# Kernel tuning notes

Measured on AMD Instinct MI355X. Metric: run time of the kernel, lower is better.

## Reference

```python
import jax, jax.numpy as jnp
import numpy as np
from jax import lax

THRESHOLD = 0.7
OUT = 224  # output size of nn.Upsample(size=(224,224), mode='bilinear', align_corners=True)


def _bilinear(img, xs, ys):
    """align_corners=True bilinear sampling. img: (..., H, W); xs: (oh,), ys: (ow,) float coords."""
    H, W = img.shape[-2], img.shape[-1]
    x0 = jnp.clip(jnp.floor(xs).astype(jnp.int32), 0, H - 1)
    x1 = jnp.clip(x0 + 1, 0, H - 1)
    y0 = jnp.clip(jnp.floor(ys).astype(jnp.int32), 0, W - 1)
    y1 = jnp.clip(y0 + 1, 0, W - 1)
    wx = (xs - x0.astype(xs.dtype))[:, None]  # (oh,1)
    wy = (ys - y0.astype(ys.dtype))[None, :]  # (1,ow)
    top = jnp.take(img, x0, axis=-2)
    bot = jnp.take(img, x1, axis=-2)
    v00 = jnp.take(top, y0, axis=-1)
    v01 = jnp.take(top, y1, axis=-1)
    v10 = jnp.take(bot, y0, axis=-1)
    v11 = jnp.take(bot, y1, axis=-1)
    return (1 - wx) * ((1 - wy) * v00 + wy * v01) + wx * ((1 - wy) * v10 + wy * v11)


def _normalize01(h):
    n = h.shape[0]
    f = h.reshape(n, -1)
    mn = f.min(axis=1, keepdims=True)
    mx = f.max(axis=1, keepdims=True)
    return ((f - mn) / (mx - mn)).reshape(h.shape)


def _largest_cc(mask):
    """8-connected (skimage connectivity=2) largest component via min-label propagation.
    mask: (N,H,W) bool -> (N,H,W) bool, True on the largest connected component."""
    N, H, W = mask.shape
    BIG = H * W  # background sentinel label
    idx = jnp.arange(BIG, dtype=jnp.int32).reshape(1, H, W)
    lab0 = jnp.where(mask, idx, BIG)

    def body(state):
        lab, _ = state
        pooled = lax.reduce_window(lab, jnp.int32(BIG), lax.min, (1, 3, 3), (1, 1, 1), 'SAME')
        new = jnp.where(mask, pooled, BIG)
        return new, jnp.any(new != lab)

    lab, _ = lax.while_loop(lambda s: s[1], body, (lab0, jnp.bool_(True)))

    def counts(l):
        return jnp.zeros(BIG + 1, jnp.int32).at[l.reshape(-1)].add(1)

    c = jax.vmap(counts)(lab)                 # (N, H*W+1); last bin = background
    best = jnp.argmax(c[:, :BIG], axis=1)     # label of largest foreground component
    return lab == best[:, None, None]


def _bbox(lcc):
    N, H, W = lcc.shape
    rows = lcc.any(axis=2)
    cols = lcc.any(axis=1)
    has = rows.any(axis=1)
    xmin = jnp.argmax(rows, axis=1).astype(jnp.int32)
    xmax = (H - 1 - jnp.argmax(rows[:, ::-1], axis=1)).astype(jnp.int32)
    ymin = jnp.argmax(cols, axis=1).astype(jnp.int32)
    ymax = (W - 1 - jnp.argmax(cols[:, ::-1], axis=1)).astype(jnp.int32)
    # fallback to full image if the mask is empty (torch code would crash here)
    xmin = jnp.where(has, xmin, 0)
    ymin = jnp.where(has, ymin, 0)
    xmax = jnp.where(has, xmax, H - 1)
    ymax = jnp.where(has, ymax, W - 1)
    return xmin, xmax, ymin, ymax


def _crop_resize(images, xmin, xmax, ymin, ymax):
    # torch crop is images[i][:, xmin:xmax, ymin:ymax] (exclusive upper), then align_corners resize
    grid = jnp.arange(OUT, dtype=jnp.float32) / (OUT - 1)

    def one(img, a, b, c, d):
        Lx = jnp.maximum(b - a, 1)
        Ly = jnp.maximum(d - c, 1)
        xs = a.astype(jnp.float32) + grid * (Lx - 1).astype(jnp.float32)
        ys = c.astype(jnp.float32) + grid * (Ly - 1).astype(jnp.float32)
        return _bilinear(img, xs, ys)

    return jax.vmap(one)(images, xmin, xmax, ymin, ymax)


def setup_inputs() -> dict:
    key = jax.random.key(0)
    k1, k2 = jax.random.split(key)
    x = jax.random.normal(k1, (64, 3, 224, 224), dtype=jnp.float32)
    features = jax.random.normal(k2, (64, 2048, 7, 7), dtype=jnp.float32)
    return {"x": x, "features": features}


def reference(x, features):
    # distance = normalize01(Lmax(features, axis=1))
    heat = _normalize01(jnp.max(jnp.abs(features), axis=1))       # (N, h, w)
    h, w = heat.shape[1], heat.shape[2]
    grid = jnp.arange(OUT, dtype=jnp.float32) / (OUT - 1)
    out_heatmap = _bilinear(heat, grid * (h - 1), grid * (w - 1))  # (N, 224, 224)
    mask = out_heatmap > THRESHOLD
    lcc = _largest_cc(mask)
    xmin, xmax, ymin, ymax = _bbox(lcc)
    crop = _crop_resize(x, xmin, xmax, ymin, ymax)                 # (N, 3, 224, 224)
    coords = jnp.stack([ymin, xmin, ymax, xmax], axis=1)           # (N, 4), torch coord order
    return crop, out_heatmap, coords
```

## Files before the change

### kernel.cpp

```cpp
#include <hip/hip_runtime.h>
#include <stdint.h>

#define NIMG   64
#define NCH    2048
#define HW7    49
#define OUTW   224
#define NPIX   50176
#define CROP_N 9633792
#define HEAT_OFF  9633792
#define COORD_OFF 12845056
#define THRESH 0.7f

#define MAXR 4
#define RCAP (224*MAXR)
#define NWORDS 784
#define WPAD   788

#define NGRP 16

#define MASKW_BYTE_OFF 262144
#define CNT_BYTE_OFF   663552

__global__ __launch_bounds__(256) void k1_heat(const float* __restrict__ F,
                                               float* __restrict__ heatPart,
                                               unsigned* __restrict__ imgCnt) {
    __shared__ float smax[4][64];
    const int t = threadIdx.x;
    const int b = blockIdx.x;
    if (b == 0 && t < NIMG) {
        __hip_atomic_store(&imgCnt[t], 0u, __ATOMIC_RELAXED, __HIP_MEMORY_SCOPE_AGENT);
    }
    const int n = b >> 4, g = b & 15;
    const int w = t >> 6, l = t & 63;
    const int lp = (l < HW7) ? l : 0;
    const float* base = F + (size_t)n * 100352 + (size_t)(g * 128 + w) * HW7 + lp;
    float vmax = 0.0f;
#pragma unroll 8
    for (int i = 0; i < 32; ++i) {
        vmax = fmaxf(vmax, fabsf(base[(size_t)i * 4 * HW7]));
    }
    smax[w][l] = vmax;
    __syncthreads();
    if (t < HW7) {
        float m = fmaxf(fmaxf(smax[0][t], smax[1][t]), fmaxf(smax[2][t], smax[3][t]));
        heatPart[b * HW7 + t] = m;
    }
}

__device__ inline unsigned uf_find(volatile unsigned* P, unsigned x) {
    while (true) {
        unsigned p = P[x];
        if (p == x) return x;
        unsigned gp = P[p];
        if (gp == p) return p;
        P[x] = gp;
        x = gp;
    }
}

__device__ inline void uf_merge(volatile unsigned* P, unsigned a, unsigned b) {
    while (true) {
        a = uf_find(P, a); b = uf_find(P, b);
        if (a == b) return;
        if (a > b) { unsigned tmp = a; a = b; b = tmp; }
        unsigned old = atomicCAS((unsigned*)&P[b], b, a);
        if (old == b) return;
        b = old;
    }
}

__global__ __launch_bounds__(1024) void k23_heatmask(const float* __restrict__ heatPart,
                                                     float* __restrict__ heatOut,
                                                     unsigned long long* __restrict__ maskW,
                                                     unsigned* __restrict__ imgCnt,
                                                     float* __restrict__ coords) {
#pragma clang fp contract(off)
    __shared__ float raw[HW7];
    __shared__ float h7[HW7];
    __shared__ float s_mn, s_mx;
    __shared__ float wT[OUTW];
    __shared__ int   i0T[OUTW];
    __shared__ int   i1T[OUTW];
    __shared__ int   s_last;
    __shared__ unsigned long long W[WPAD];
    __shared__ unsigned short runS[RCAP], runE[RCAP];
    __shared__ unsigned char nRuns[224];
    __shared__ unsigned parent[RCAP], cnt[RCAP];
    __shared__ unsigned rmin[RCAP], rmax[RCAP], cmin[RCAP], cmax[RCAP];
    __shared__ unsigned bestScore, bestRid;

    const int t = threadIdx.x;
    const int b = blockIdx.x;
    const int n = b >> 2, slice = b & 3;

    if (t < HW7) {
        float m = heatPart[(n * NGRP + 0) * HW7 + t];
#pragma unroll
        for (int g = 1; g < NGRP; ++g) m = fmaxf(m, heatPart[(n * NGRP + g) * HW7 + t]);
        raw[t] = m;
    }
    if (t < OUTW) {
        float gx = (float)t / 223.0f;
        float xs = gx * 6.0f;
        int x0 = (int)floorf(xs); x0 = min(max(x0, 0), 6);
        i0T[t] = x0;
        i1T[t] = min(x0 + 1, 6);
        wT[t]  = xs - (float)x0;
    }
    __syncthreads();
    if (t == 0) {
        float mn = raw[0], mx = raw[0];
        for (int i = 1; i < HW7; ++i) { float v = raw[i]; mn = fminf(mn, v); mx = fmaxf(mx, v); }
        s_mn = mn; s_mx = mx;
    }
    __syncthreads();
    if (t < HW7) h7[t] = (raw[t] - s_mn) / (s_mx - s_mn);
    __syncthreads();

    const int pbase = slice * 12544;
    for (int k = 0; k < 13; ++k) {
        int pl = (k << 10) + t;
        if (pl < 12544) {
            int p = pbase + pl;
            int i = p / 224, j = p - i * 224;
            int x0 = i0T[i], x1 = i1T[i];
            int y0 = i0T[j], y1 = i1T[j];
            float wx = wT[i], wy = wT[j];
            float v00 = h7[x0 * 7 + y0], v01 = h7[x0 * 7 + y1];
            float v10 = h7[x1 * 7 + y0], v11 = h7[x1 * 7 + y1];
            float val = (1.0f - wx) * ((1.0f - wy) * v00 + wy * v01)
                      + wx * ((1.0f - wy) * v10 + wy * v11);
            heatOut[(size_t)n * NPIX + p] = val;
            unsigned long long bal = __ballot(val > THRESH);
            if ((t & 63) == 0) {
                __hip_atomic_store(&maskW[(size_t)n * NWORDS + (p >> 6)], bal,
                                   __ATOMIC_RELAXED, __HIP_MEMORY_SCOPE_AGENT);
            }
        }
    }

    __syncthreads();
    if (t == 0) {
        unsigned old = __hip_atomic_fetch_add(&imgCnt[n], 1u,
                                              __ATOMIC_ACQ_REL, __HIP_MEMORY_SCOPE_AGENT);
        s_last = (old == 3u);
    }
    __syncthreads();
    if (!s_last) return;

    if (t < NWORDS) W[t] = __hip_atomic_load(&maskW[(size_t)n * NWORDS + t],
                                             __ATOMIC_RELAXED, __HIP_MEMORY_SCOPE_AGENT);
    if (t >= NWORDS && t < WPAD) W[t] = 0ull;
    if (t < RCAP) {
        parent[t] = (unsigned)t; cnt[t] = 0u;
        rmin[t] = 0xFFFFFFFFu; rmax[t] = 0u; cmin[t] = 0xFFFFFFFFu; cmax[t] = 0u;
    }
    if (t == 0) { bestScore = 0u; bestRid = 0u; }
    __syncthreads();

    if (t < 224) {
        const int r = t;
        const int bit0 = r * 224;
        const int w0 = bit0 >> 6, sh = bit0 & 63;
        unsigned long long rb[4];
#pragma unroll
        for (int q = 0; q < 4; ++q) {
            unsigned long long lo = W[w0 + q] >> sh;
            unsigned long long hi = sh ? (W[w0 + q + 1] << (64 - sh)) : 0ull;
            rb[q] = lo | hi;
        }
        rb[3] &= 0xFFFFFFFFull;

        unsigned long long st[4], en[4];
        unsigned long long carry = 0ull;
#pragma unroll
        for (int q = 0; q < 4; ++q) {
            unsigned long long shl = (rb[q] << 1) | carry;
            carry = rb[q] >> 63;
            st[q] = rb[q] & ~shl;
        }
#pragma unroll
        for (int q = 0; q < 4; ++q) {
            unsigned long long nxt = (q < 3) ? rb[q + 1] : 0ull;
            en[q] = rb[q] & ~((rb[q] >> 1) | (nxt << 63));
        }
        int ns = 0;
#pragma unroll
        for (int q = 0; q < 4; ++q) {
            unsigned long long x = st[q];
            while (x) {
                int z = __builtin_ctzll(x); x &= x - 1;
                if (ns < MAXR) runS[r * MAXR + ns] = (unsigned short)(q * 64 + z);
                ns++;
            }
        }
        int ne = 0;
#pragma unroll
        for (int q = 0; q < 4; ++q) {
            unsigned long long x = en[q];
            while (x) {
                int z = __builtin_ctzll(x); x &= x - 1;
                if (ne < MAXR) runE[r * MAXR + ne] = (unsigned short)(q * 64 + z);
                ne++;
            }
        }
        nRuns[r] = (unsigned char)min(ns, MAXR);
    }
    __syncthreads();

    if (t >= MAXR && t < RCAP) {
        const int r = t >> 2, k = t & (MAXR - 1);
        if (k < (int)nRuns[r]) {
            const int nb = nRuns[r - 1];
            int s = runS[t], e = runE[t];
            for (int m = 0; m < nb; ++m) {
                int qid = (r - 1) * MAXR + m;
                int s2 = runS[qid], e2 = runE[qid];
                if (s2 <= e + 1 && e2 >= s - 1) uf_merge(parent, (unsigned)t, (unsigned)qid);
            }
        }
    }
    __syncthreads();

    if (t < RCAP) {
        int r = t >> 2, k = t & (MAXR - 1);
        if (k < (int)nRuns[r]) {
            int s = runS[t], e = runE[t];
            unsigned root = uf_find(parent, (unsigned)t);
            atomicAdd(&cnt[root], (unsigned)(e - s + 1));
            atomicMin(&rmin[root], (unsigned)r);
            atomicMax(&rmax[root], (unsigned)r);
            atomicMin(&cmin[root], (unsigned)s);
            atomicMax(&cmax[root], (unsigned)e);
        }
    }
    __syncthreads();

    if (t < RCAP) {
        unsigned c = cnt[t];
        if (c > 0u) {
            unsigned label = (unsigned)((t >> 2) * 224 + (int)runS[t]);
            unsigned score = (c << 16) | (65535u - label);
            atomicMax(&bestScore, score);
        }
    }
    __syncthreads();
    if (t < RCAP) {
        unsigned c = cnt[t];
        if (c > 0u) {
            unsigned label = (unsigned)((t >> 2) * 224 + (int)runS[t]);
            unsigned score = (c << 16) | (65535u - label);
            if (score == bestScore) bestRid = (unsigned)t;
        }
    }
    __syncthreads();

    if (t == 0) {
        int xmin, xmax, ymin, ymax;
        if (bestScore == 0u) {
            xmin = 0; ymin = 0; xmax = 223; ymax = 223;
        } else {
            unsigned rb_ = bestRid;
            xmin = (int)rmin[rb_]; xmax = (int)rmax[rb_];
            ymin = (int)cmin[rb_]; ymax = (int)cmax[rb_];
        }
        coords[n * 4 + 0] = (float)ymin;
        coords[n * 4 + 1] = (float)xmin;
        coords[n * 4 + 2] = (float)ymax;
        coords[n * 4 + 3] = (float)xmax;
    }
}

__global__ __launch_bounds__(256) void k4_crop(const float* __restrict__ X,
                                               const float* __restrict__ coords,
                                               float* __restrict__ out) {
#pragma clang fp contract(off)
    const int t = threadIdx.x;
    const int b = blockIdx.x;
    const int n = b / 49;
    const int p4 = ((b % 49) * 256 + t) * 4;
    const int oi = p4 / 224, oj = p4 - oi * 224;

    int ymin = (int)coords[n * 4 + 0];
    int xmin = (int)coords[n * 4 + 1];
    int ymax = (int)coords[n * 4 + 2];
    int xmax = (int)coords[n * 4 + 3];
    int Lx = max(xmax - xmin, 1);
    int Ly = max(ymax - ymin, 1);

    float gx = (float)oi / 223.0f;
    float xs = (float)xmin + gx * (float)(Lx - 1);
    int x0 = (int)floorf(xs); x0 = min(max(x0, 0), 223); int x1 = min(x0 + 1, 223);
    float wx = xs - (float)x0;

    int   y0q[4], y1q[4];
    float wyq[4];
#pragma unroll
    for (int q = 0; q < 4; ++q) {
        float gy = (float)(oj + q) / 223.0f;
        float ys = (float)ymin + gy * (float)(Ly - 1);
        int y0 = (int)floorf(ys); y0 = min(max(y0, 0), 223);
        y0q[q] = y0; y1q[q] = min(y0 + 1, 223);
        wyq[q] = ys - (float)y0;
    }

    const float* img = X + (size_t)n * 150528;
    float* obase = out + (size_t)n * 150528 + p4;
#pragma unroll
    for (int ch = 0; ch < 3; ++ch) {
        const float* rt = img + ch * NPIX + x0 * 224;
        const float* rb = img + ch * NPIX + x1 * 224;
        float r[4];
#pragma unroll
        for (int q = 0; q < 4; ++q) {
            float v00 = rt[y0q[q]], v01 = rt[y1q[q]];
            float v10 = rb[y0q[q]], v11 = rb[y1q[q]];
            r[q] = (1.0f - wx) * ((1.0f - wyq[q]) * v00 + wyq[q] * v01)
                 + wx * ((1.0f - wyq[q]) * v10 + wyq[q] * v11);
        }
        *reinterpret_cast<float4*>(obase + (size_t)ch * NPIX) =
            make_float4(r[0], r[1], r[2], r[3]);
    }
}

extern "C" void kernel_launch(void* const* d_in, const int* in_sizes, int n_in,
                              void* d_out, int out_size, void* d_ws, size_t ws_size,
                              hipStream_t stream) {
    (void)in_sizes; (void)n_in; (void)out_size; (void)d_ws; (void)ws_size;
    const float* X = (const float*)d_in[0];
    const float* F = (const float*)d_in[1];
    float* out = (float*)d_out;

    float* heatPart = (float*)d_out;
    unsigned long long* maskW = (unsigned long long*)((char*)d_out + MASKW_BYTE_OFF);
    unsigned* imgCnt = (unsigned*)((char*)d_out + CNT_BYTE_OFF);
    float* heatOut = out + HEAT_OFF;
    float* coords  = out + COORD_OFF;

    k1_heat     <<<dim3(1024), dim3(256),  0, stream>>>(F, heatPart, imgCnt);
    k23_heatmask<<<dim3(256),  dim3(1024), 0, stream>>>(heatPart, heatOut, maskW, imgCnt, coords);
    k4_crop     <<<dim3(3136), dim3(256),  0, stream>>>(X, coords, out);
}
```

Measured before the change: 137.5 us.

## Fuse heatmap, connected-component and crop stages into one kernel with flag sync

Merges the heat/mask kernel and the crop-resize kernel into a single 256-block kernel. The last block per image computes the bbox and publishes a flag, and the other three slice blocks spin-wait on that flag before doing their share of the crop. Scratch buffers move from the output buffer to the workspace when one is available, and the old three-kernel path is kept as a fallback. This removes one kernel launch and its boundary, but adds a spin-wait that assumes all 256 blocks of 1024 threads are co-resident, and the crop runs on only 256 blocks instead of 3136.

```diff
diff --git a/kernel.cpp b/kernel.cpp
--- a/kernel.cpp
+++ b/kernel.cpp
@@ -18,8 +18,13 @@
 
 #define NGRP 16
 
-#define MASKW_BYTE_OFF 262144
-#define CNT_BYTE_OFF   663552
+#define WS_HP_OFF    0
+#define WS_MW_OFF    200704
+#define WS_CNT_OFF   602112
+#define WS_NEEDED    602624
+
+#define FB_MASKW_BYTE_OFF 262144
+#define FB_CNT_BYTE_OFF   663552
 
 __global__ __launch_bounds__(256) void k1_heat(const float* __restrict__ F,
                                                float* __restrict__ heatPart,
@@ -27,7 +32,7 @@
     __shared__ float smax[4][64];
     const int t = threadIdx.x;
     const int b = blockIdx.x;
-    if (b == 0 && t < NIMG) {
+    if (b == 0 && t < 128) {
         __hip_atomic_store(&imgCnt[t], 0u, __ATOMIC_RELAXED, __HIP_MEMORY_SCOPE_AGENT);
     }
     const int n = b >> 4, g = b & 15;
@@ -66,6 +71,275 @@
         unsigned old = atomicCAS((unsigned*)&P[b], b, a);
         if (old == b) return;
         b = old;
+    }
+}
+
+__global__ __launch_bounds__(1024) void k234(const float* __restrict__ heatPart,
+                                             const float* __restrict__ X,
+                                             unsigned long long* __restrict__ maskW,
+                                             unsigned* __restrict__ cnt1,
+                                             unsigned* __restrict__ flag,
+                                             float* heatOut,
+                                             float* coords,
+                                             float* out) {
+#pragma clang fp contract(off)
+    __shared__ float raw[HW7];
+    __shared__ float h7[HW7];
+    __shared__ float s_mn, s_mx;
+    __shared__ float wT[OUTW];
+    __shared__ int   i0T[OUTW];
+    __shared__ int   i1T[OUTW];
+    __shared__ int   s_last;
+    __shared__ unsigned long long W[WPAD];
+    __shared__ unsigned short runS[RCAP], runE[RCAP];
+    __shared__ unsigned char nRuns[224];
+    __shared__ unsigned parent[RCAP], cnt[RCAP];
+    __shared__ unsigned rmin[RCAP], rmax[RCAP], cmin[RCAP], cmax[RCAP];
+    __shared__ unsigned bestScore, bestRid;
+    __shared__ float s_crd[4];
+
+    const int t = threadIdx.x;
+    const int b = blockIdx.x;
+    const int n = b >> 2, slice = b & 3;
+
+    if (t < HW7) {
+        float m = heatPart[(n * NGRP + 0) * HW7 + t];
+#pragma unroll
+        for (int g = 1; g < NGRP; ++g) m = fmaxf(m, heatPart[(n * NGRP + g) * HW7 + t]);
+        raw[t] = m;
+    }
+    if (t < OUTW) {
+        float gx = (float)t / 223.0f;
+        float xs = gx * 6.0f;
+        int x0 = (int)floorf(xs); x0 = min(max(x0, 0), 6);
+        i0T[t] = x0;
+        i1T[t] = min(x0 + 1, 6);
+        wT[t]  = xs - (float)x0;
+    }
+    __syncthreads();
+    if (t == 0) {
+        float mn = raw[0], mx = raw[0];
+        for (int i = 1; i < HW7; ++i) { float v = raw[i]; mn = fminf(mn, v); mx = fmaxf(mx, v); }
+        s_mn = mn; s_mx = mx;
+    }
+    __syncthreads();
+    if (t < HW7) h7[t] = (raw[t] - s_mn) / (s_mx - s_mn);
+    __syncthreads();
+
+    const int pbase = slice * 12544;
+    for (int k = 0; k < 13; ++k) {
+        int pl = (k << 10) + t;
+        if (pl < 12544) {
+            int p = pbase + pl;
+            int i = p / 224, j = p - i * 224;
+            int x0 = i0T[i], x1 = i1T[i];
+            int y0 = i0T[j], y1 = i1T[j];
+            float wx = wT[i], wy = wT[j];
+            float v00 = h7[x0 * 7 + y0], v01 = h7[x0 * 7 + y1];
+            float v10 = h7[x1 * 7 + y0], v11 = h7[x1 * 7 + y1];
+            float val = (1.0f - wx) * ((1.0f - wy) * v00 + wy * v01)
+                      + wx * ((1.0f - wy) * v10 + wy * v11);
+            heatOut[(size_t)n * NPIX + p] = val;
+            unsigned long long bal = __ballot(val > THRESH);
+            if ((t & 63) == 0) {
+                __hip_atomic_store(&maskW[(size_t)n * NWORDS + (p >> 6)], bal,
+                                   __ATOMIC_RELAXED, __HIP_MEMORY_SCOPE_AGENT);
+            }
+        }
+    }
+
+    __syncthreads();
+    if (t == 0) {
+        unsigned old = __hip_atomic_fetch_add(&cnt1[n], 1u,
+                                              __ATOMIC_ACQ_REL, __HIP_MEMORY_SCOPE_AGENT);
+        s_last = (old == 3u);
+    }
+    __syncthreads();
+
+    if (s_last) {
+        if (t < NWORDS) W[t] = __hip_atomic_load(&maskW[(size_t)n * NWORDS + t],
+                                                 __ATOMIC_RELAXED, __HIP_MEMORY_SCOPE_AGENT);
+        if (t >= NWORDS && t < WPAD) W[t] = 0ull;
+        if (t < RCAP) {
+            parent[t] = (unsigned)t; cnt[t] = 0u;
+            rmin[t] = 0xFFFFFFFFu; rmax[t] = 0u; cmin[t] = 0xFFFFFFFFu; cmax[t] = 0u;
+        }
+        if (t == 0) { bestScore = 0u; bestRid = 0u; }
+        __syncthreads();
+
+        if (t < 224) {
+            const int r = t;
+            const int bit0 = r * 224;
+            const int w0 = bit0 >> 6, sh = bit0 & 63;
+            unsigned long long rb[4];
+#pragma unroll
+            for (int q = 0; q < 4; ++q) {
+                unsigned long long lo = W[w0 + q] >> sh;
+                unsigned long long hi = sh ? (W[w0 + q + 1] << (64 - sh)) : 0ull;
+                rb[q] = lo | hi;
+            }
+            rb[3] &= 0xFFFFFFFFull;
+
+            unsigned long long st[4], en[4];
+            unsigned long long carry = 0ull;
+#pragma unroll
+            for (int q = 0; q < 4; ++q) {
+                unsigned long long shl = (rb[q] << 1) | carry;
+                carry = rb[q] >> 63;
+                st[q] = rb[q] & ~shl;
+            }
+#pragma unroll
+            for (int q = 0; q < 4; ++q) {
+                unsigned long long nxt = (q < 3) ? rb[q + 1] : 0ull;
+                en[q] = rb[q] & ~((rb[q] >> 1) | (nxt << 63));
+            }
+            int ns = 0;
+#pragma unroll
+            for (int q = 0; q < 4; ++q) {
+                unsigned long long x = st[q];
+                while (x) {
+                    int z = __builtin_ctzll(x); x &= x - 1;
+                    if (ns < MAXR) runS[r * MAXR + ns] = (unsigned short)(q * 64 + z);
+                    ns++;
+                }
+            }
+            int ne = 0;
+#pragma unroll
+            for (int q = 0; q < 4; ++q) {
+                unsigned long long x = en[q];
+                while (x) {
+                    int z = __builtin_ctzll(x); x &= x - 1;
+                    if (ne < MAXR) runE[r * MAXR + ne] = (unsigned short)(q * 64 + z);
+                    ne++;
+                }
+            }
+            nRuns[r] = (unsigned char)min(ns, MAXR);
+        }
+        __syncthreads();
+
+        if (t >= MAXR && t < RCAP) {
+            const int r = t >> 2, k = t & (MAXR - 1);
+            if (k < (int)nRuns[r]) {
+                const int nb = nRuns[r - 1];
+                int s = runS[t], e = runE[t];
+                for (int m = 0; m < nb; ++m) {
+                    int qid = (r - 1) * MAXR + m;
+                    int s2 = runS[qid], e2 = runE[qid];
+                    if (s2 <= e + 1 && e2 >= s - 1) uf_merge(parent, (unsigned)t, (unsigned)qid);
+                }
+            }
+        }
+        __syncthreads();
+
+        if (t < RCAP) {
+            int r = t >> 2, k = t & (MAXR - 1);
+            if (k < (int)nRuns[r]) {
+                int s = runS[t], e = runE[t];
+                unsigned root = uf_find(parent, (unsigned)t);
+                atomicAdd(&cnt[root], (unsigned)(e - s + 1));
+                atomicMin(&rmin[root], (unsigned)r);
+                atomicMax(&rmax[root], (unsigned)r);
+                atomicMin(&cmin[root], (unsigned)s);
+                atomicMax(&cmax[root], (unsigned)e);
+            }
+        }
+        __syncthreads();
+
+        if (t < RCAP) {
+            unsigned c = cnt[t];
+            if (c > 0u) {
+                unsigned label = (unsigned)((t >> 2) * 224 + (int)runS[t]);
+                unsigned score = (c << 16) | (65535u - label);
+                atomicMax(&bestScore, score);
+            }
+        }
+        __syncthreads();
+        if (t < RCAP) {
+            unsigned c = cnt[t];
+            if (c > 0u) {
+                unsigned label = (unsigned)((t >> 2) * 224 + (int)runS[t]);
+                unsigned score = (c << 16) | (65535u - label);
+                if (score == bestScore) bestRid = (unsigned)t;
+            }
+        }
+        __syncthreads();
+
+        if (t == 0) {
+            int xmin, xmax, ymin, ymax;
+            if (bestScore == 0u) {
+                xmin = 0; ymin = 0; xmax = 223; ymax = 223;
+            } else {
+                unsigned rb_ = bestRid;
+                xmin = (int)rmin[rb_]; xmax = (int)rmax[rb_];
+                ymin = (int)cmin[rb_]; ymax = (int)cmax[rb_];
+            }
+            __hip_atomic_store(&coords[n * 4 + 0], (float)ymin, __ATOMIC_RELAXED, __HIP_MEMORY_SCOPE_AGENT);
+            __hip_atomic_store(&coords[n * 4 + 1], (float)xmin, __ATOMIC_RELAXED, __HIP_MEMORY_SCOPE_AGENT);
+            __hip_atomic_store(&coords[n * 4 + 2], (float)ymax, __ATOMIC_RELAXED, __HIP_MEMORY_SCOPE_AGENT);
+            __hip_atomic_store(&coords[n * 4 + 3], (float)xmax, __ATOMIC_RELAXED, __HIP_MEMORY_SCOPE_AGENT);
+            __hip_atomic_store(&flag[n], 1u, __ATOMIC_RELEASE, __HIP_MEMORY_SCOPE_AGENT);
+        }
+    }
+
+    if (t == 0) {
+        while (__hip_atomic_load(&flag[n], __ATOMIC_ACQUIRE, __HIP_MEMORY_SCOPE_AGENT) == 0u) {
+            __builtin_amdgcn_s_sleep(2);
+        }
+    }
+    __syncthreads();
+    if (t < 4) s_crd[t] = __hip_atomic_load(&coords[n * 4 + t],
+                                            __ATOMIC_RELAXED, __HIP_MEMORY_SCOPE_AGENT);
+    __syncthreads();
+
+    {
+        const int ymin = (int)s_crd[0];
+        const int xmin = (int)s_crd[1];
+        const int ymax = (int)s_crd[2];
+        const int xmax = (int)s_crd[3];
+        const int Lx = max(xmax - xmin, 1);
+        const int Ly = max(ymax - ymin, 1);
+        const float* img = X + (size_t)n * 150528;
+
+        for (int iter = 0; iter < 4; ++iter) {
+            int loc = (iter << 10) + t;
+            if (loc < 3136) {
+                int p4 = (slice * 3136 + loc) * 4;
+                int oi = p4 / 224, oj = p4 - oi * 224;
+
+                float gx = (float)oi / 223.0f;
+                float xs = (float)xmin + gx * (float)(Lx - 1);
+                int x0 = (int)floorf(xs); x0 = min(max(x0, 0), 223); int x1 = min(x0 + 1, 223);
+                float wx = xs - (float)x0;
+
+                int   y0q[4], y1q[4];
+                float wyq[4];
+#pragma unroll
+                for (int q = 0; q < 4; ++q) {
+                    float gy = (float)(oj + q) / 223.0f;
+                    float ys = (float)ymin + gy * (float)(Ly - 1);
+                    int y0 = (int)floorf(ys); y0 = min(max(y0, 0), 223);
+                    y0q[q] = y0; y1q[q] = min(y0 + 1, 223);
+                    wyq[q] = ys - (float)y0;
+                }
+
+                float* obase = out + (size_t)n * 150528 + p4;
+#pragma unroll
+                for (int ch = 0; ch < 3; ++ch) {
+                    const float* rt = img + ch * NPIX + x0 * 224;
+                    const float* rb = img + ch * NPIX + x1 * 224;
+                    float r[4];
+#pragma unroll
+                    for (int q = 0; q < 4; ++q) {
+                        float v00 = rt[y0q[q]], v01 = rt[y1q[q]];
+                        float v10 = rb[y0q[q]], v11 = rb[y1q[q]];
+                        r[q] = (1.0f - wx) * ((1.0f - wyq[q]) * v00 + wyq[q] * v01)
+                             + wx * ((1.0f - wyq[q]) * v10 + wyq[q] * v11);
+                    }
+                    *reinterpret_cast<float4*>(obase + (size_t)ch * NPIX) =
+                        make_float4(r[0], r[1], r[2], r[3]);
+                }
+            }
+        }
     }
 }
 
@@ -170,7 +444,6 @@
             rb[q] = lo | hi;
         }
         rb[3] &= 0xFFFFFFFFull;
-
         unsigned long long st[4], en[4];
         unsigned long long carry = 0ull;
 #pragma unroll
@@ -326,18 +599,29 @@
 extern "C" void kernel_launch(void* const* d_in, const int* in_sizes, int n_in,
                               void* d_out, int out_size, void* d_ws, size_t ws_size,
                               hipStream_t stream) {
-    (void)in_sizes; (void)n_in; (void)out_size; (void)d_ws; (void)ws_size;
+    (void)in_sizes; (void)n_in; (void)out_size;
     const float* X = (const float*)d_in[0];
     const float* F = (const float*)d_in[1];
     float* out = (float*)d_out;
-
-    float* heatPart = (float*)d_out;
-    unsigned long long* maskW = (unsigned long long*)((char*)d_out + MASKW_BYTE_OFF);
-    unsigned* imgCnt = (unsigned*)((char*)d_out + CNT_BYTE_OFF);
     float* heatOut = out + HEAT_OFF;
     float* coords  = out + COORD_OFF;
 
-    k1_heat     <<<dim3(1024), dim3(256),  0, stream>>>(F, heatPart, imgCnt);
-    k23_heatmask<<<dim3(256),  dim3(1024), 0, stream>>>(heatPart, heatOut, maskW, imgCnt, coords);
-    k4_crop     <<<dim3(3136), dim3(256),  0, stream>>>(X, coords, out);
+    if (d_ws != nullptr && ws_size >= (size_t)WS_NEEDED) {
+        float* heatPart = (float*)((char*)d_ws + WS_HP_OFF);
+        unsigned long long* maskW = (unsigned long long*)((char*)d_ws + WS_MW_OFF);
+        unsigned* cnt1 = (unsigned*)((char*)d_ws + WS_CNT_OFF);
+        unsigned* flag = cnt1 + 64;
+
+        k1_heat<<<dim3(1024), dim3(256),  0, stream>>>(F, heatPart, cnt1);
+        k234   <<<dim3(256),  dim3(1024), 0, stream>>>(heatPart, X, maskW, cnt1, flag,
+                                                       heatOut, coords, out);
+    } else {
+        float* heatPart = (float*)d_out;
+        unsigned long long* maskW = (unsigned long long*)((char*)d_out + FB_MASKW_BYTE_OFF);
+        unsigned* imgCnt = (unsigned*)((char*)d_out + FB_CNT_BYTE_OFF);
+
+        k1_heat     <<<dim3(1024), dim3(256),  0, stream>>>(F, heatPart, imgCnt);
+        k23_heatmask<<<dim3(256),  dim3(1024), 0, stream>>>(heatPart, heatOut, maskW, imgCnt, coords);
+        k4_crop     <<<dim3(3136), dim3(256),  0, stream>>>(X, coords, out);
+    }
 }
```

New measurement: 145.8 us. +6.1%, slower.
